# Kernel optimization log

Hardware: AMD Instinct MI355X
Metric: run time of the kernel (lower is better)

Reference implementation:

```python
import jax, jax.numpy as jnp
import numpy as np

N_NODES = 50000
N_EDGES = 800000
N_FEAT = 128
HIDDEN = 128
N_GRAPHS = 256


def gcn_conv(x, W, b, src, dst, n_nodes):
    # PyG GCNConv, add_self_loops=False, edge_weight=1:
    # out_i = sum_{(j->i)} d_j^{-1/2} d_i^{-1/2} (x_j @ W) + b, deg over target idx
    h = x @ W                                    # [N, out]
    deg = jax.ops.segment_sum(jnp.ones((src.shape[0],), h.dtype), dst,
                              num_segments=n_nodes)          # [N]
    dis = jnp.where(deg > 0, jax.lax.rsqrt(jnp.maximum(deg, 1.0)), 0.0)
    norm = dis[src] * dis[dst]                   # [E]
    msg = h[src] * norm[:, None]                 # [E, out] gather + scale
    out = jax.ops.segment_sum(msg, dst, num_segments=n_nodes)  # scatter-add
    return out + b


def setup_inputs() -> dict:
    key = jax.random.key(0)
    ks = jax.random.split(key, 12)
    x = jax.random.normal(ks[0], (N_NODES, N_FEAT), jnp.float32)
    edge_index = jax.random.randint(ks[1], (2, N_EDGES), 0, N_NODES, jnp.int64)
    batch = jnp.sort(jax.random.randint(ks[2], (N_NODES,), 0, N_GRAPHS, jnp.int64))

    def glorot(k, shape):
        lim = float(np.sqrt(6.0 / (shape[0] + shape[1])))
        return jax.random.uniform(k, shape, jnp.float32, -lim, lim)

    W1 = glorot(ks[3], (N_FEAT, HIDDEN)); b1 = jnp.zeros((HIDDEN,), jnp.float32)
    W2 = glorot(ks[4], (HIDDEN, HIDDEN)); b2 = jnp.zeros((HIDDEN,), jnp.float32)
    Wf1 = glorot(ks[5], (HIDDEN, HIDDEN // 2)); bf1 = jnp.zeros((HIDDEN // 2,), jnp.float32)
    Wl = glorot(ks[6], (HIDDEN // 2, 2)); bl = jnp.zeros((2,), jnp.float32)
    return {"x": x, "edge_index": edge_index, "batch": batch,
            "W1": W1, "b1": b1, "W2": W2, "b2": b2,
            "Wf1": Wf1, "bf1": bf1, "Wl": Wl, "bl": bl}


def reference(x, edge_index, batch, W1, b1, W2, b2, Wf1, bf1, Wl, bl):
    src, dst = edge_index[0], edge_index[1]
    h = jax.nn.relu(gcn_conv(x, W1, b1, src, dst, N_NODES))
    h = jax.nn.relu(gcn_conv(h, W2, b2, src, dst, N_NODES))
    h = gcn_conv(h, W2, b2, src, dst, N_NODES)   # conv2 applied a second time (same weights)
    # global_mean_pool over graphs
    sums = jax.ops.segment_sum(h, batch, num_segments=N_GRAPHS)      # [G, H]
    cnts = jax.ops.segment_sum(jnp.ones((h.shape[0],), h.dtype), batch,
                               num_segments=N_GRAPHS)                # [G]
    g = sums / jnp.maximum(cnts, 1.0)[:, None]
    g = jax.nn.relu(g @ Wf1 + bf1)
    logits = g @ Wl + bl
    return jax.nn.softmax(logits, axis=1)
```

## Files before the change

### kernel.cpp

```cpp
#include <hip/hip_runtime.h>
#include <hip/hip_bf16.h>

#define N_NODES 50000
#define N_EDGES 800000
#define NF 128
#define NG 256
#define CAP 64
#define NSEG 256
#define SEGE (N_EDGES / NSEG)
#define NPAD 50048

typedef unsigned short ushort_t;
typedef unsigned char uchar_t;
typedef __attribute__((ext_vector_type(8))) short bf16x8;
typedef __attribute__((ext_vector_type(4))) float f32x4;

__device__ __forceinline__ float b2f(ushort_t u) {
    union { unsigned i; float f; } x; x.i = ((unsigned)u) << 16; return x.f;
}
__device__ __forceinline__ ushort_t f2b(float f) {
    union { float f; unsigned i; } x; x.f = f;
    unsigned r = (x.i + 0x7fffu + ((x.i >> 16) & 1u)) >> 16;
    return (ushort_t)r;
}

__global__ __launch_bounds__(512) void k_seg_count(
        const int* __restrict__ dst, uchar_t* __restrict__ segcnt,
        float* __restrict__ gsum) {
    __shared__ unsigned int cntw[NPAD / 4];
    int tid = threadIdx.x;
    int b = blockIdx.x;
    if (b < 16) {
        ((float4*)gsum)[b * 512 + tid] = make_float4(0.f, 0.f, 0.f, 0.f);
    }
    for (int i = tid; i < NPAD / 4; i += 512) cntw[i] = 0;
    __syncthreads();
    const int* d0 = dst + b * SEGE;
    for (int e = tid; e < SEGE; e += 512) {
        int d = d0[e];
        atomicAdd(&cntw[d >> 2], 1u << ((d & 3) * 8));
    }
    __syncthreads();
    unsigned int* outw = (unsigned int*)(segcnt + (size_t)b * NPAD);
    for (int i = tid; i < NPAD / 4; i += 512) outw[i] = cntw[i];
}

__global__ void k_seg_scan(const uchar_t* __restrict__ segcnt,
                           uchar_t* __restrict__ segbase,
                           int* __restrict__ deg, float* __restrict__ dis) {
    int node = blockIdx.x * 256 + threadIdx.x;
    if (node >= N_NODES) return;
    int run = 0;
    for (int s = 0; s < NSEG; ++s) {
        size_t idx = (size_t)s * NPAD + node;
        int c = segcnt[idx];
        segbase[idx] = (uchar_t)min(run, 255);
        run += c;
    }
    deg[node] = min(run, CAP);
    dis[node] = (run > 0) ? rsqrtf((float)run) : 0.f;
}

__global__ __launch_bounds__(512) void k_seg_fill(
        const int* __restrict__ src, const int* __restrict__ dst,
        const uchar_t* __restrict__ segbase, ushort_t* __restrict__ csr_pad) {
    __shared__ unsigned int cntw[NPAD / 4];
    int tid = threadIdx.x;
    int b = blockIdx.x;
    for (int i = tid; i < NPAD / 4; i += 512) cntw[i] = 0;
    __syncthreads();
    const int* d0 = dst + b * SEGE;
    const int* s0 = src + b * SEGE;
    const uchar_t* brow = segbase + (size_t)b * NPAD;
    for (int e = tid; e < SEGE; e += 512) {
        int d = d0[e];
        int sh = (d & 3) * 8;
        unsigned old = atomicAdd(&cntw[d >> 2], 1u << sh);
        int pos = (old >> sh) & 0xFF;
        int slot = brow[d] + pos;
        if (slot < CAP) csr_pad[(size_t)d * CAP + slot] = (ushort_t)s0[e];
    }
}

__global__ void k_prep_w2(const float* __restrict__ W1, const float* __restrict__ W2,
                          ushort_t* __restrict__ W1h, ushort_t* __restrict__ W1l,
                          ushort_t* __restrict__ W2h, ushort_t* __restrict__ W2l) {
    int t = blockIdx.x * blockDim.x + threadIdx.x;
    int which = t >> 14;
    int u = t & 16383;
    int k = u >> 7, c = u & 127;
    const float* W = which ? W2 : W1;
    ushort_t* Wh = which ? W2h : W1h;
    ushort_t* Wl = which ? W2l : W1l;
    float w = W[k * 128 + c];
    ushort_t hi = f2b(w);
    ushort_t lo = f2b(w - b2f(hi));
    Wh[c * 128 + k] = hi;
    Wl[c * 128 + k] = lo;
}

template <bool F32A>
__global__ __launch_bounds__(256) void k_gemm_mfma(
        const float* __restrict__ Xf, const ushort_t* __restrict__ Xb,
        const ushort_t* __restrict__ Wt_hi, const ushort_t* __restrict__ Wt_lo,
        const float* __restrict__ dis, ushort_t* __restrict__ Yb, int n) {
    __shared__ ushort_t Wlds[2][16384];
    int t = threadIdx.x;
    {
        const int4* gh = (const int4*)Wt_hi;
        const int4* gl = (const int4*)Wt_lo;
        int4* sh = (int4*)&Wlds[0][0];
        int4* sl = (int4*)&Wlds[1][0];
#pragma unroll
        for (int i = 0; i < 8; ++i) {
            int u = t + i * 256;
            int swz = u ^ ((u >> 4) & 7);
            sh[swz] = gh[u];
            sl[swz] = gl[u];
        }
    }
    __syncthreads();

    int wid = t >> 6;
    int l   = t & 63;
    int la  = l & 15;
    int kb  = l >> 4;
    int r0  = blockIdx.x * 64 + wid * 16;

    bf16x8 a[4];
    {
        int ra = min(r0 + la, n - 1);
        if (F32A) {
            const float* xrow = Xf + (size_t)ra * 128 + kb * 8;
#pragma unroll
            for (int kt = 0; kt < 4; ++kt) {
                float4 v0 = *(const float4*)(xrow + kt * 32);
                float4 v1 = *(const float4*)(xrow + kt * 32 + 4);
                bf16x8 av;
                av[0] = (short)f2b(v0.x); av[1] = (short)f2b(v0.y);
                av[2] = (short)f2b(v0.z); av[3] = (short)f2b(v0.w);
                av[4] = (short)f2b(v1.x); av[5] = (short)f2b(v1.y);
                av[6] = (short)f2b(v1.z); av[7] = (short)f2b(v1.w);
                a[kt] = av;
            }
        } else {
            const ushort_t* xrow = Xb + (size_t)ra * 128 + kb * 8;
#pragma unroll
            for (int kt = 0; kt < 4; ++kt)
                a[kt] = *(const bf16x8*)(xrow + kt * 32);
        }
    }

    f32x4 acc[8];
#pragma unroll
    for (int ct = 0; ct < 8; ++ct) acc[ct] = (f32x4){0.f, 0.f, 0.f, 0.f};

#pragma unroll
    for (int ct = 0; ct < 8; ++ct) {
        int c = ct * 16 + la;
        int ubase = c * 128 + kb * 8;
        int sw = (c & 7) << 3;
#pragma unroll
        for (int kt = 0; kt < 4; ++kt) {
            int u16 = (ubase + kt * 32) ^ sw;
            bf16x8 bh = *(const bf16x8*)&Wlds[0][u16];
            bf16x8 bl = *(const bf16x8*)&Wlds[1][u16];
            acc[ct] = __builtin_amdgcn_mfma_f32_16x16x32_bf16(a[kt], bh, acc[ct], 0, 0, 0);
            acc[ct] = __builtin_amdgcn_mfma_f32_16x16x32_bf16(a[kt], bl, acc[ct], 0, 0, 0);
        }
    }

    float dsc[4];
#pragma unroll
    for (int j = 0; j < 4; ++j)
        dsc[j] = dis[min(r0 + kb * 4 + j, n - 1)];

    __syncthreads();
    ushort_t* tile = ((ushort_t*)Wlds) + wid * 2048;
#pragma unroll
    for (int ct = 0; ct < 8; ++ct) {
        int cc = ct * 16 + la;
#pragma unroll
        for (int j = 0; j < 4; ++j)
            tile[(kb * 4 + j) * 128 + cc] = f2b(acc[ct][j] * dsc[j]);
    }
    __syncthreads();
    {
        const int4* t4 = (const int4*)tile;
        int4* dst4 = (int4*)(Yb + (size_t)r0 * 128);
#pragma unroll
        for (int i = 0; i < 4; ++i) {
            int u = l * 4 + i;
            int row = u >> 4;
            if (r0 + row < n) dst4[u] = t4[u];
        }
    }
}

template <bool RELU>
__global__ __launch_bounds__(256) void k_agg(
        const ushort_t* __restrict__ Hs, const int* __restrict__ deg,
        const ushort_t* __restrict__ csr_pad, const float* __restrict__ dis,
        const float* __restrict__ bias, ushort_t* __restrict__ out, int n) {
    int lane = threadIdx.x & 31;
    int sub  = threadIdx.x >> 5;
    int node = blockIdx.x * 8 + sub;
    if (node >= n) return;
    int dg = deg[node];
    const ushort_t* lst = csr_pad + (size_t)node * CAP;
    int c0 = lane * 4;

    float4 a0 = make_float4(0.f, 0.f, 0.f, 0.f);
    float4 a1 = make_float4(0.f, 0.f, 0.f, 0.f);
    float4 a2 = make_float4(0.f, 0.f, 0.f, 0.f);
    float4 a3 = make_float4(0.f, 0.f, 0.f, 0.f);
    int p = 0;
    for (; p + 3 < dg; p += 4) {
        int j0 = lst[p], j1 = lst[p + 1], j2 = lst[p + 2], j3 = lst[p + 3];
        ushort4 v0 = *(const ushort4*)&Hs[(size_t)j0 * 128 + c0];
        ushort4 v1 = *(const ushort4*)&Hs[(size_t)j1 * 128 + c0];
        ushort4 v2 = *(const ushort4*)&Hs[(size_t)j2 * 128 + c0];
        ushort4 v3 = *(const ushort4*)&Hs[(size_t)j3 * 128 + c0];
        a0.x += b2f(v0.x); a0.y += b2f(v0.y); a0.z += b2f(v0.z); a0.w += b2f(v0.w);
        a1.x += b2f(v1.x); a1.y += b2f(v1.y); a1.z += b2f(v1.z); a1.w += b2f(v1.w);
        a2.x += b2f(v2.x); a2.y += b2f(v2.y); a2.z += b2f(v2.z); a2.w += b2f(v2.w);
        a3.x += b2f(v3.x); a3.y += b2f(v3.y); a3.z += b2f(v3.z); a3.w += b2f(v3.w);
    }
    for (; p < dg; ++p) {
        int j = lst[p];
        ushort4 v = *(const ushort4*)&Hs[(size_t)j * 128 + c0];
        a0.x += b2f(v.x); a0.y += b2f(v.y); a0.z += b2f(v.z); a0.w += b2f(v.w);
    }
    float dsc = dis[node];
    float4 b = *(const float4*)&bias[c0];
    float rx = ((a0.x + a1.x) + (a2.x + a3.x)) * dsc + b.x;
    float ry = ((a0.y + a1.y) + (a2.y + a3.y)) * dsc + b.y;
    float rz = ((a0.z + a1.z) + (a2.z + a3.z)) * dsc + b.z;
    float rw = ((a0.w + a1.w) + (a2.w + a3.w)) * dsc + b.w;
    if (RELU) {
        rx = fmaxf(rx, 0.f); ry = fmaxf(ry, 0.f);
        rz = fmaxf(rz, 0.f); rw = fmaxf(rw, 0.f);
    }
    ushort4 o;
    o.x = f2b(rx); o.y = f2b(ry); o.z = f2b(rz); o.w = f2b(rw);
    *(ushort4*)&out[(size_t)node * 128 + c0] = o;
}

#define POOL_CHUNK 128
__global__ __launch_bounds__(128) void k_pool_partial(
        const ushort_t* __restrict__ H, const int* __restrict__ batch,
        float* __restrict__ gsum, int n) {
    int f = threadIdx.x;
    int s = blockIdx.x * POOL_CHUNK;
    int e = min(s + POOL_CHUNK, n);
    if (s >= n) return;
    float acc = 0.f;
    int g = batch[s];
    for (int i = s; i < e; ++i) {
        int bg = batch[i];
        if (bg != g) {
            atomicAdd(&gsum[g * 128 + f], acc);
            acc = 0.f;
            g = bg;
        }
        acc += b2f(H[(size_t)i * 128 + f]);
    }
    atomicAdd(&gsum[g * 128 + f], acc);
}

__global__ void k_head(const float* __restrict__ gsum, const int* __restrict__ batch,
                       const float* __restrict__ Wf1, const float* __restrict__ bf1,
                       const float* __restrict__ Wl, const float* __restrict__ bl,
                       float* __restrict__ out, int n) {
    int g = blockIdx.x;
    int j = threadIdx.x;
    __shared__ float xs[128];
    __shared__ float hs[64];

    int lo = 0, hi = n;
    while (lo < hi) { int m = (lo + hi) >> 1; if (batch[m] < g) lo = m + 1; else hi = m; }
    int s0 = lo;
    hi = n;
    while (lo < hi) { int m = (lo + hi) >> 1; if (batch[m] <= g) lo = m + 1; else hi = m; }
    float inv_cnt = 1.f / fmaxf((float)(lo - s0), 1.f);

    xs[j]      = gsum[g * 128 + j] * inv_cnt;
    xs[j + 64] = gsum[g * 128 + 64 + j] * inv_cnt;
    __syncthreads();
    float acc = bf1[j];
#pragma unroll 4
    for (int k = 0; k < 128; k++) acc += xs[k] * Wf1[k * 64 + j];
    hs[j] = fmaxf(acc, 0.f);
    __syncthreads();
    if (j == 0) {
        float l0 = bl[0], l1 = bl[1];
        for (int k = 0; k < 64; k++) { l0 += hs[k] * Wl[k * 2 + 0]; l1 += hs[k] * Wl[k * 2 + 1]; }
        float m  = fmaxf(l0, l1);
        float e0 = expf(l0 - m), e1 = expf(l1 - m);
        float inv = 1.f / (e0 + e1);
        out[g * 2 + 0] = e0 * inv;
        out[g * 2 + 1] = e1 * inv;
    }
}

extern "C" void kernel_launch(void* const* d_in, const int* in_sizes, int n_in,
                              void* d_out, int out_size, void* d_ws, size_t ws_size,
                              hipStream_t stream) {
    const float* x    = (const float*)d_in[0];
    const int*   eidx = (const int*)d_in[1];
    const int*   batch= (const int*)d_in[2];
    const float* W1   = (const float*)d_in[3];
    const float* b1   = (const float*)d_in[4];
    const float* W2   = (const float*)d_in[5];
    const float* b2   = (const float*)d_in[6];
    const float* Wf1  = (const float*)d_in[7];
    const float* bf1  = (const float*)d_in[8];
    const float* Wl   = (const float*)d_in[9];
    const float* bl   = (const float*)d_in[10];
    float* out = (float*)d_out;

    const int* src = eidx;
    const int* dst = eidx + N_EDGES;

    char* w = (char*)d_ws;
    auto alloc = [&](size_t bytes) -> void* {
        void* p = (void*)w;
        w += (bytes + 255) & ~(size_t)255;
        return p;
    };
    ushort_t* Yb     = (ushort_t*)alloc((size_t)N_NODES * NF * 2);
    ushort_t* Hb     = (ushort_t*)alloc((size_t)N_NODES * NF * 2);
    ushort_t* W1h    = (ushort_t*)alloc((size_t)NF * NF * 2);
    ushort_t* W1l    = (ushort_t*)alloc((size_t)NF * NF * 2);
    ushort_t* W2h    = (ushort_t*)alloc((size_t)NF * NF * 2);
    ushort_t* W2l    = (ushort_t*)alloc((size_t)NF * NF * 2);
    float*    dis    = (float*)alloc((size_t)N_NODES * 4);
    int*      deg    = (int*)  alloc((size_t)N_NODES * 4);
    ushort_t* csr_pad= (ushort_t*)alloc((size_t)N_NODES * CAP * 2);
    uchar_t*  segcnt = (uchar_t*)alloc((size_t)NSEG * NPAD);
    uchar_t*  segbase= (uchar_t*)alloc((size_t)NSEG * NPAD);
    float*    gsum   = (float*)alloc((size_t)NG * NF * 4);

    k_seg_count<<<NSEG, 512, 0, stream>>>(dst, segcnt, gsum);
    k_seg_scan<<<(N_NODES + 255) / 256, 256, 0, stream>>>(segcnt, segbase, deg, dis);
    k_seg_fill<<<NSEG, 512, 0, stream>>>(src, dst, segbase, csr_pad);

    k_prep_w2<<<128, 256, 0, stream>>>(W1, W2, W1h, W1l, W2h, W2l);

    int gb = (N_NODES + 63) / 64;
    int ab = (N_NODES + 7) / 8;
    k_gemm_mfma<true><<<gb, 256, 0, stream>>>(x, nullptr, W1h, W1l, dis, Yb, N_NODES);
    k_agg<true><<<ab, 256, 0, stream>>>(Yb, deg, csr_pad, dis, b1, Hb, N_NODES);
    k_gemm_mfma<false><<<gb, 256, 0, stream>>>(nullptr, Hb, W2h, W2l, dis, Yb, N_NODES);
    k_agg<true><<<ab, 256, 0, stream>>>(Yb, deg, csr_pad, dis, b2, Hb, N_NODES);
    k_gemm_mfma<false><<<gb, 256, 0, stream>>>(nullptr, Hb, W2h, W2l, dis, Yb, N_NODES);
    k_agg<false><<<ab, 256, 0, stream>>>(Yb, deg, csr_pad, dis, b2, Hb, N_NODES);

    k_pool_partial<<<(N_NODES + POOL_CHUNK - 1) / POOL_CHUNK, 128, 0, stream>>>(Hb, batch, gsum, N_NODES);
    k_head<<<NG, 64, 0, stream>>>(gsum, batch, Wf1, bf1, Wl, bl, out, N_NODES);
}
```

Before: 237.9 us.

## Fuse weight prep into count kernel, retile GEMM by columns, unroll aggregation by 8

The weight hi/lo bf16 split now runs in extra blocks of the segment-count kernel, which removes one kernel launch. The MFMA GEMM now has each wave cover all 64 rows for a 32-column slice, so each LDS weight fragment is reused across four row tiles. The output is staged in fp32 LDS, and the dis scaling is applied during a coalesced write-out. The aggregation loop is unrolled to 8 neighbors with 8 accumulators to keep more loads in flight, at the cost of more registers.

```diff
diff --git a/kernel.cpp b/kernel.cpp
--- a/kernel.cpp
+++ b/kernel.cpp
@@ -9,6 +9,7 @@
 #define NSEG 256
 #define SEGE (N_EDGES / NSEG)
 #define NPAD 50048
+#define NPREP 64
 
 typedef unsigned short ushort_t;
 typedef unsigned char uchar_t;
@@ -26,10 +27,28 @@
 
 __global__ __launch_bounds__(512) void k_seg_count(
         const int* __restrict__ dst, uchar_t* __restrict__ segcnt,
-        float* __restrict__ gsum) {
+        float* __restrict__ gsum,
+        const float* __restrict__ W1, const float* __restrict__ W2,
+        ushort_t* __restrict__ W1h, ushort_t* __restrict__ W1l,
+        ushort_t* __restrict__ W2h, ushort_t* __restrict__ W2l) {
     __shared__ unsigned int cntw[NPAD / 4];
     int tid = threadIdx.x;
     int b = blockIdx.x;
+    if (b >= NSEG) {
+        int id = (b - NSEG) * 512 + tid;
+        int which = id >> 14;
+        int u = id & 16383;
+        int k = u >> 7, c = u & 127;
+        const float* W = which ? W2 : W1;
+        ushort_t* Wh = which ? W2h : W1h;
+        ushort_t* Wl = which ? W2l : W1l;
+        float w = W[k * 128 + c];
+        ushort_t hi = f2b(w);
+        ushort_t lo = f2b(w - b2f(hi));
+        Wh[c * 128 + k] = hi;
+        Wl[c * 128 + k] = lo;
+        return;
+    }
     if (b < 16) {
         ((float4*)gsum)[b * 512 + tid] = make_float4(0.f, 0.f, 0.f, 0.f);
     }
@@ -80,23 +99,6 @@
         int slot = brow[d] + pos;
         if (slot < CAP) csr_pad[(size_t)d * CAP + slot] = (ushort_t)s0[e];
     }
-}
-
-__global__ void k_prep_w2(const float* __restrict__ W1, const float* __restrict__ W2,
-                          ushort_t* __restrict__ W1h, ushort_t* __restrict__ W1l,
-                          ushort_t* __restrict__ W2h, ushort_t* __restrict__ W2l) {
-    int t = blockIdx.x * blockDim.x + threadIdx.x;
-    int which = t >> 14;
-    int u = t & 16383;
-    int k = u >> 7, c = u & 127;
-    const float* W = which ? W2 : W1;
-    ushort_t* Wh = which ? W2h : W1h;
-    ushort_t* Wl = which ? W2l : W1l;
-    float w = W[k * 128 + c];
-    ushort_t hi = f2b(w);
-    ushort_t lo = f2b(w - b2f(hi));
-    Wh[c * 128 + k] = hi;
-    Wl[c * 128 + k] = lo;
 }
 
 template <bool F32A>
@@ -125,11 +127,13 @@
     int l   = t & 63;
     int la  = l & 15;
     int kb  = l >> 4;
-    int r0  = blockIdx.x * 64 + wid * 16;
-
-    bf16x8 a[4];
-    {
-        int ra = min(r0 + la, n - 1);
+    int r0  = blockIdx.x * 64;
+    int cw  = wid * 32;
+
+    bf16x8 a[4][4];
+#pragma unroll
+    for (int rt = 0; rt < 4; ++rt) {
+        int ra = min(r0 + rt * 16 + la, n - 1);
         if (F32A) {
             const float* xrow = Xf + (size_t)ra * 128 + kb * 8;
 #pragma unroll
@@ -141,23 +145,25 @@
                 av[2] = (short)f2b(v0.z); av[3] = (short)f2b(v0.w);
                 av[4] = (short)f2b(v1.x); av[5] = (short)f2b(v1.y);
                 av[6] = (short)f2b(v1.z); av[7] = (short)f2b(v1.w);
-                a[kt] = av;
+                a[rt][kt] = av;
             }
         } else {
             const ushort_t* xrow = Xb + (size_t)ra * 128 + kb * 8;
 #pragma unroll
             for (int kt = 0; kt < 4; ++kt)
-                a[kt] = *(const bf16x8*)(xrow + kt * 32);
-        }
-    }
-
-    f32x4 acc[8];
-#pragma unroll
-    for (int ct = 0; ct < 8; ++ct) acc[ct] = (f32x4){0.f, 0.f, 0.f, 0.f};
-
-#pragma unroll
-    for (int ct = 0; ct < 8; ++ct) {
-        int c = ct * 16 + la;
+                a[rt][kt] = *(const bf16x8*)(xrow + kt * 32);
+        }
+    }
+
+    f32x4 acc[4][2];
+#pragma unroll
+    for (int rt = 0; rt < 4; ++rt)
+#pragma unroll
+        for (int ct = 0; ct < 2; ++ct) acc[rt][ct] = (f32x4){0.f, 0.f, 0.f, 0.f};
+
+#pragma unroll
+    for (int ct = 0; ct < 2; ++ct) {
+        int c = cw + ct * 16 + la;
         int ubase = c * 128 + kb * 8;
         int sw = (c & 7) << 3;
 #pragma unroll
@@ -165,34 +171,42 @@
             int u16 = (ubase + kt * 32) ^ sw;
             bf16x8 bh = *(const bf16x8*)&Wlds[0][u16];
             bf16x8 bl = *(const bf16x8*)&Wlds[1][u16];
-            acc[ct] = __builtin_amdgcn_mfma_f32_16x16x32_bf16(a[kt], bh, acc[ct], 0, 0, 0);
-            acc[ct] = __builtin_amdgcn_mfma_f32_16x16x32_bf16(a[kt], bl, acc[ct], 0, 0, 0);
-        }
-    }
-
-    float dsc[4];
-#pragma unroll
-    for (int j = 0; j < 4; ++j)
-        dsc[j] = dis[min(r0 + kb * 4 + j, n - 1)];
-
-    __syncthreads();
-    ushort_t* tile = ((ushort_t*)Wlds) + wid * 2048;
-#pragma unroll
-    for (int ct = 0; ct < 8; ++ct) {
-        int cc = ct * 16 + la;
-#pragma unroll
-        for (int j = 0; j < 4; ++j)
-            tile[(kb * 4 + j) * 128 + cc] = f2b(acc[ct][j] * dsc[j]);
+#pragma unroll
+            for (int rt = 0; rt < 4; ++rt) {
+                acc[rt][ct] = __builtin_amdgcn_mfma_f32_16x16x32_bf16(a[rt][kt], bh, acc[rt][ct], 0, 0, 0);
+                acc[rt][ct] = __builtin_amdgcn_mfma_f32_16x16x32_bf16(a[rt][kt], bl, acc[rt][ct], 0, 0, 0);
+            }
+        }
+    }
+
+    __syncthreads();
+    float* tile = (float*)Wlds;
+#pragma unroll
+    for (int rt = 0; rt < 4; ++rt) {
+#pragma unroll
+        for (int ct = 0; ct < 2; ++ct) {
+            int cc = cw + ct * 16 + la;
+#pragma unroll
+            for (int j = 0; j < 4; ++j)
+                tile[(rt * 16 + kb * 4 + j) * 128 + cc] = acc[rt][ct][j];
+        }
     }
     __syncthreads();
     {
-        const int4* t4 = (const int4*)tile;
-        int4* dst4 = (int4*)(Yb + (size_t)r0 * 128);
-#pragma unroll
-        for (int i = 0; i < 4; ++i) {
-            int u = l * 4 + i;
-            int row = u >> 4;
-            if (r0 + row < n) dst4[u] = t4[u];
+        const float4* t4 = (const float4*)tile;
+#pragma unroll
+        for (int i = 0; i < 8; ++i) {
+            int u = t + i * 256;
+            int row = u >> 5;
+            int r = r0 + row;
+            if (r < n) {
+                float4 v = t4[u];
+                float s = dis[r];
+                ushort4 o;
+                o.x = f2b(v.x * s); o.y = f2b(v.y * s);
+                o.z = f2b(v.z * s); o.w = f2b(v.w * s);
+                ((ushort4*)(Yb + (size_t)r * 128))[u & 31] = o;
+            }
         }
     }
 }
@@ -214,7 +228,31 @@
     float4 a1 = make_float4(0.f, 0.f, 0.f, 0.f);
     float4 a2 = make_float4(0.f, 0.f, 0.f, 0.f);
     float4 a3 = make_float4(0.f, 0.f, 0.f, 0.f);
+    float4 a4 = make_float4(0.f, 0.f, 0.f, 0.f);
+    float4 a5 = make_float4(0.f, 0.f, 0.f, 0.f);
+    float4 a6 = make_float4(0.f, 0.f, 0.f, 0.f);
+    float4 a7 = make_float4(0.f, 0.f, 0.f, 0.f);
     int p = 0;
+    for (; p + 7 < dg; p += 8) {
+        int j0 = lst[p],     j1 = lst[p + 1], j2 = lst[p + 2], j3 = lst[p + 3];
+        int j4 = lst[p + 4], j5 = lst[p + 5], j6 = lst[p + 6], j7 = lst[p + 7];
+        ushort4 v0 = *(const ushort4*)&Hs[(size_t)j0 * 128 + c0];
+        ushort4 v1 = *(const ushort4*)&Hs[(size_t)j1 * 128 + c0];
+        ushort4 v2 = *(const ushort4*)&Hs[(size_t)j2 * 128 + c0];
+        ushort4 v3 = *(const ushort4*)&Hs[(size_t)j3 * 128 + c0];
+        ushort4 v4 = *(const ushort4*)&Hs[(size_t)j4 * 128 + c0];
+        ushort4 v5 = *(const ushort4*)&Hs[(size_t)j5 * 128 + c0];
+        ushort4 v6 = *(const ushort4*)&Hs[(size_t)j6 * 128 + c0];
+        ushort4 v7 = *(const ushort4*)&Hs[(size_t)j7 * 128 + c0];
+        a0.x += b2f(v0.x); a0.y += b2f(v0.y); a0.z += b2f(v0.z); a0.w += b2f(v0.w);
+        a1.x += b2f(v1.x); a1.y += b2f(v1.y); a1.z += b2f(v1.z); a1.w += b2f(v1.w);
+        a2.x += b2f(v2.x); a2.y += b2f(v2.y); a2.z += b2f(v2.z); a2.w += b2f(v2.w);
+        a3.x += b2f(v3.x); a3.y += b2f(v3.y); a3.z += b2f(v3.z); a3.w += b2f(v3.w);
+        a4.x += b2f(v4.x); a4.y += b2f(v4.y); a4.z += b2f(v4.z); a4.w += b2f(v4.w);
+        a5.x += b2f(v5.x); a5.y += b2f(v5.y); a5.z += b2f(v5.z); a5.w += b2f(v5.w);
+        a6.x += b2f(v6.x); a6.y += b2f(v6.y); a6.z += b2f(v6.z); a6.w += b2f(v6.w);
+        a7.x += b2f(v7.x); a7.y += b2f(v7.y); a7.z += b2f(v7.z); a7.w += b2f(v7.w);
+    }
     for (; p + 3 < dg; p += 4) {
         int j0 = lst[p], j1 = lst[p + 1], j2 = lst[p + 2], j3 = lst[p + 3];
         ushort4 v0 = *(const ushort4*)&Hs[(size_t)j0 * 128 + c0];
@@ -233,10 +271,10 @@
     }
     float dsc = dis[node];
     float4 b = *(const float4*)&bias[c0];
-    float rx = ((a0.x + a1.x) + (a2.x + a3.x)) * dsc + b.x;
-    float ry = ((a0.y + a1.y) + (a2.y + a3.y)) * dsc + b.y;
-    float rz = ((a0.z + a1.z) + (a2.z + a3.z)) * dsc + b.z;
-    float rw = ((a0.w + a1.w) + (a2.w + a3.w)) * dsc + b.w;
+    float rx = (((a0.x + a1.x) + (a2.x + a3.x)) + ((a4.x + a5.x) + (a6.x + a7.x))) * dsc + b.x;
+    float ry = (((a0.y + a1.y) + (a2.y + a3.y)) + ((a4.y + a5.y) + (a6.y + a7.y))) * dsc + b.y;
+    float rz = (((a0.z + a1.z) + (a2.z + a3.z)) + ((a4.z + a5.z) + (a6.z + a7.z))) * dsc + b.z;
+    float rw = (((a0.w + a1.w) + (a2.w + a3.w)) + ((a4.w + a5.w) + (a6.w + a7.w))) * dsc + b.w;
     if (RELU) {
         rx = fmaxf(rx, 0.f); ry = fmaxf(ry, 0.f);
         rz = fmaxf(rz, 0.f); rw = fmaxf(rw, 0.f);
@@ -341,11 +379,10 @@
     uchar_t*  segbase= (uchar_t*)alloc((size_t)NSEG * NPAD);
     float*    gsum   = (float*)alloc((size_t)NG * NF * 4);
 
-    k_seg_count<<<NSEG, 512, 0, stream>>>(dst, segcnt, gsum);
+    k_seg_count<<<NSEG + NPREP, 512, 0, stream>>>(dst, segcnt, gsum,
+                                                  W1, W2, W1h, W1l, W2h, W2l);
     k_seg_scan<<<(N_NODES + 255) / 256, 256, 0, stream>>>(segcnt, segbase, deg, dis);
     k_seg_fill<<<NSEG, 512, 0, stream>>>(src, dst, segbase, csr_pad);
-
-    k_prep_w2<<<128, 256, 0, stream>>>(W1, W2, W1h, W1l, W2h, W2l);
 
     int gb = (N_NODES + 63) / 64;
     int ab = (N_NODES + 7) / 8;
```

Result: slower. 249.6 us (+4.9%).
